# Optimization experiments

Hardware: AMD Instinct MI355X
Metric: run time of the kernel (lower is better)

The kernel has to match this reference:

```python
import jax, jax.numpy as jnp
import numpy as np


def _gcn_conv(x, src, dst, dis, W, b, num_nodes):
    # x: [N, Fin]; src/dst: [E+N] (self-loops included); dis: [N] deg^{-1/2}
    h = x @ W                                   # [N, Fout] dense transform first (Fin >= Fout)
    norm = dis[src] * dis[dst]                  # [E+N] symmetric GCN normalization
    msg = h[src] * norm[:, None]                # gather + scale
    out = jax.ops.segment_sum(msg, dst, num_segments=num_nodes)  # scatter-add at targets
    return out + b


def setup_inputs() -> dict:
    key = jax.random.key(0)
    k1, k2, k3, k4 = jax.random.split(key, 4)
    N, F, H, C, E = 100000, 512, 32, 32, 3200000
    x = jax.random.normal(k1, (N, F), dtype=jnp.float32)
    edge_index = jax.random.randint(k2, (2, E), 0, N, dtype=jnp.int64)
    W1 = jax.random.normal(k3, (F, H), dtype=jnp.float32) * (1.0 / np.sqrt(F))
    b1 = jnp.zeros((H,), dtype=jnp.float32)
    W2 = jax.random.normal(k4, (H, C), dtype=jnp.float32) * (1.0 / np.sqrt(H))
    b2 = jnp.zeros((C,), dtype=jnp.float32)
    return {"x": x, "edge_index": edge_index, "W1": W1, "b1": b1, "W2": W2, "b2": b2}


def reference(x, edge_index, W1, b1, W2, b2):
    N = x.shape[0]
    loop = jnp.arange(N, dtype=edge_index.dtype)
    src = jnp.concatenate([edge_index[0], loop])   # add self-loops (PyG default)
    dst = jnp.concatenate([edge_index[1], loop])
    deg = jax.ops.segment_sum(jnp.ones_like(dst, dtype=x.dtype), dst, num_segments=N)
    dis = jnp.where(deg > 0, jax.lax.rsqrt(jnp.maximum(deg, 1.0)), 0.0)  # deg^{-1/2}, 0 for isolated
    h = _gcn_conv(x, src, dst, dis, W1, b1, N)
    h = jax.nn.relu(h)                              # dropout is identity in eval mode
    h = _gcn_conv(h, src, dst, dis, W2, b2, N)
    return jax.nn.log_softmax(h, axis=1)
```

## Files before the change

### kernel.cpp

```cpp
#include <hip/hip_runtime.h>
#include <hip/hip_bf16.h>

#define FIN 512
#define HD 32
#define BNODES 512
#define CH 8192
#define NHB 128

typedef short s16x8 __attribute__((ext_vector_type(8)));
typedef float f32x4 __attribute__((ext_vector_type(4)));

__device__ inline unsigned short f2b(float f) {
  unsigned u = __float_as_uint(f);
  return (unsigned short)((u + 0x7FFFu + ((u >> 16) & 1u)) >> 16);
}
__device__ inline float b2f(unsigned short b) {
  return __uint_as_float((unsigned)b << 16);
}
__device__ inline float b2f_lo(unsigned u) { return __uint_as_float(u << 16); }
__device__ inline float b2f_hi(unsigned u) { return __uint_as_float(u & 0xFFFF0000u); }

__global__ __launch_bounds__(256) void k_bktcnt(const int* __restrict__ dst, int* __restrict__ hist, int E) {
  __shared__ int h[256];
  int t = threadIdx.x;
  h[t] = 0;
  __syncthreads();
  for (int i = blockIdx.x * 256 + t; i < E; i += gridDim.x * 256)
    atomicAdd(&h[dst[i] >> 9], 1);
  __syncthreads();
  hist[blockIdx.x * 256 + t] = h[t];
}

__global__ __launch_bounds__(256) void k_bscan(const int* __restrict__ hist, int* __restrict__ bcnt,
                                               int* __restrict__ bbase, int* __restrict__ bfill) {
  __shared__ int s[256];
  int t = threadIdx.x;
  int v = 0;
  for (int b = 0; b < NHB; ++b) v += hist[b * 256 + t];
  bcnt[t] = v;
  s[t] = v;
  __syncthreads();
  for (int o = 1; o < 256; o <<= 1) {
    int a = (t >= o) ? s[t - o] : 0;
    __syncthreads();
    s[t] += a;
    __syncthreads();
  }
  bbase[t] = s[t] - v;
  bfill[t] = s[t] - v;
}

__global__ __launch_bounds__(512) void k_bin(const int* __restrict__ src, const int* __restrict__ dst,
                                             int* __restrict__ bfill, int* __restrict__ bin, int E) {
  __shared__ int raw[CH];
  __shared__ unsigned char bkt[CH];
  __shared__ int cnt[256];
  __shared__ int gbase[256];
  int t = threadIdx.x;
  for (int cb = blockIdx.x * CH; cb < E; cb += gridDim.x * CH) {
    int n = E - cb; if (n > CH) n = CH;
    if (t < 256) cnt[t] = 0;
    __syncthreads();
    for (int j = t; j < n; j += 512) {
      int s = src[cb + j], d = dst[cb + j];
      raw[j] = s | ((d & 511) << 22);
      bkt[j] = (unsigned char)(d >> 9);
      atomicAdd(&cnt[d >> 9], 1);
    }
    __syncthreads();
    if (t < 256) {
      int c = cnt[t];
      gbase[t] = (c > 0) ? atomicAdd(&bfill[t], c) : 0;
      cnt[t] = 0;
    }
    __syncthreads();
    for (int j = t; j < n; j += 512) {
      int b = bkt[j];
      int r = atomicAdd(&cnt[b], 1);
      bin[gbase[b] + r] = raw[j];
    }
    __syncthreads();
  }
}

__global__ __launch_bounds__(512) void k_csr(const int* __restrict__ bin, const int* __restrict__ bbase,
                                             const int* __restrict__ bcnt, int* __restrict__ cntm1,
                                             float* __restrict__ dis, int* __restrict__ offsets,
                                             int* __restrict__ csr, int N) {
  __shared__ int cnt[BNODES];
  __shared__ int sc[BNODES];
  const int t = threadIdx.x;
  const int bkt = blockIdx.x;
  const int n0 = bkt * BNODES;
  int nn = N - n0; if (nn > BNODES) nn = BNODES;
  const int eb = bbase[bkt], ec = bcnt[bkt];

  cnt[t] = 0;
  __syncthreads();
  for (int j = t; j < ec; j += 512)
    atomicAdd(&cnt[(unsigned)bin[eb + j] >> 22], 1);
  __syncthreads();
  int v = cnt[t];
  if (t < nn) {
    cntm1[n0 + t] = v;
    dis[n0 + t] = rsqrtf((float)(v + 1));
  }
  sc[t] = v;
  __syncthreads();
  for (int o = 1; o < 512; o <<= 1) {
    int a = (t >= o) ? sc[t - o] : 0;
    __syncthreads();
    sc[t] += a;
    __syncthreads();
  }
  int myoff = sc[t] - v;
  if (t < nn) offsets[n0 + t] = eb + myoff;
  cnt[t] = myoff;
  __syncthreads();
  for (int j = t; j < ec; j += 512) {
    int e = bin[eb + j];
    int pos = atomicAdd(&cnt[(unsigned)e >> 22], 1);
    csr[eb + pos] = e & 0x3FFFFF;
  }
}

#define XPAD 72
#define WPAD 520
__global__ __launch_bounds__(512) void k_mm1(const float* __restrict__ x, const float* __restrict__ W1,
                                             const float* __restrict__ dis, unsigned short* __restrict__ h1b,
                                             int N) {
  __shared__ unsigned short wT[32 * WPAD];
  __shared__ unsigned short xs[128 * XPAD];
  const int t = threadIdx.x;
  const int rbase = blockIdx.x * 128;

  for (int idx = t; idx < FIN * HD; idx += 512) {
    int k = idx >> 5, c = idx & 31;
    wT[c * WPAD + k] = f2b(W1[idx]);
  }

  const int lane = t & 63;
  const int wrow = (t >> 6) * 16;
  const int m16 = lane & 15;
  const int kg = lane >> 4;

  f32x4 acc0 = {0.f, 0.f, 0.f, 0.f};
  f32x4 acc1 = {0.f, 0.f, 0.f, 0.f};

  for (int kc = 0; kc < FIN; kc += 64) {
    __syncthreads();
#pragma unroll
    for (int p = 0; p < 4; ++p) {
      int idx = p * 512 + t;
      int r = idx >> 4, kq = idx & 15;
      int grow = rbase + r;
      float4 v = (grow < N) ? *(const float4*)&x[(size_t)grow * FIN + kc + kq * 4]
                            : make_float4(0.f, 0.f, 0.f, 0.f);
      unsigned p0 = (unsigned)f2b(v.x) | ((unsigned)f2b(v.y) << 16);
      unsigned p1 = (unsigned)f2b(v.z) | ((unsigned)f2b(v.w) << 16);
      *(uint2*)&xs[r * XPAD + kq * 4] = make_uint2(p0, p1);
    }
    __syncthreads();

    s16x8 a0  = *(const s16x8*)&xs[(wrow + m16) * XPAD + kg * 8];
    s16x8 a1  = *(const s16x8*)&xs[(wrow + m16) * XPAD + 32 + kg * 8];
    s16x8 b00 = *(const s16x8*)&wT[m16 * WPAD + kc + kg * 8];
    s16x8 b01 = *(const s16x8*)&wT[(16 + m16) * WPAD + kc + kg * 8];
    s16x8 b10 = *(const s16x8*)&wT[m16 * WPAD + kc + 32 + kg * 8];
    s16x8 b11 = *(const s16x8*)&wT[(16 + m16) * WPAD + kc + 32 + kg * 8];
    acc0 = __builtin_amdgcn_mfma_f32_16x16x32_bf16(a0, b00, acc0, 0, 0, 0);
    acc1 = __builtin_amdgcn_mfma_f32_16x16x32_bf16(a0, b01, acc1, 0, 0, 0);
    acc0 = __builtin_amdgcn_mfma_f32_16x16x32_bf16(a1, b10, acc0, 0, 0, 0);
    acc1 = __builtin_amdgcn_mfma_f32_16x16x32_bf16(a1, b11, acc1, 0, 0, 0);
  }

#pragma unroll
  for (int r = 0; r < 4; ++r) {
    int row = rbase + wrow + kg * 4 + r;
    if (row < N) {
      float dr = dis[row];
      h1b[(size_t)row * HD + m16]      = f2b(acc0[r] * dr);
      h1b[(size_t)row * HD + 16 + m16] = f2b(acc1[r] * dr);
    }
  }
}

__device__ inline float pull_row(const unsigned short* __restrict__ h, const int* __restrict__ csr,
                                 int jb, int cnt, int L, int es, int cg) {
  float a0 = 0.f, a1 = 0.f, a2 = 0.f, a3 = 0.f, a4 = 0.f, a5 = 0.f, a6 = 0.f, a7 = 0.f;
  for (int j = 0; j < cnt; j += 8) {
    int eidx = j + es;
    int sidx = csr[jb + min(eidx, cnt - 1)];
    uint4 u = *(const uint4*)&h[(size_t)sidx * HD + cg * 8];
    if (eidx >= cnt) u = make_uint4(0, 0, 0, 0);
    a0 += b2f_lo(u.x); a1 += b2f_hi(u.x);
    a2 += b2f_lo(u.y); a3 += b2f_hi(u.y);
    a4 += b2f_lo(u.z); a5 += b2f_hi(u.z);
    a6 += b2f_lo(u.w); a7 += b2f_hi(u.w);
  }
#pragma unroll
  for (int o = 4; o <= 16; o <<= 1) {
    a0 += __shfl_xor(a0, o, 32); a1 += __shfl_xor(a1, o, 32);
    a2 += __shfl_xor(a2, o, 32); a3 += __shfl_xor(a3, o, 32);
    a4 += __shfl_xor(a4, o, 32); a5 += __shfl_xor(a5, o, 32);
    a6 += __shfl_xor(a6, o, 32); a7 += __shfl_xor(a7, o, 32);
  }
  int srcl = L >> 3;
  int sel = L & 7;
  float sum = __shfl(a0, srcl, 32);
  float c1 = __shfl(a1, srcl, 32); sum = (sel == 1) ? c1 : sum;
  float c2 = __shfl(a2, srcl, 32); sum = (sel == 2) ? c2 : sum;
  float c3 = __shfl(a3, srcl, 32); sum = (sel == 3) ? c3 : sum;
  float c4 = __shfl(a4, srcl, 32); sum = (sel == 4) ? c4 : sum;
  float c5 = __shfl(a5, srcl, 32); sum = (sel == 5) ? c5 : sum;
  float c6 = __shfl(a6, srcl, 32); sum = (sel == 6) ? c6 : sum;
  float c7 = __shfl(a7, srcl, 32); sum = (sel == 7) ? c7 : sum;
  return sum;
}

__global__ __launch_bounds__(256) void k_pull1_mm2(const unsigned short* __restrict__ h1b,
                                                   const int* __restrict__ csr, const int* __restrict__ offsets,
                                                   const int* __restrict__ cntm1, const float* __restrict__ dis,
                                                   const float* __restrict__ b1, const float* __restrict__ W2,
                                                   unsigned short* __restrict__ h2b, int N) {
  __shared__ float w[HD * HD];
  __shared__ float bb[HD];
  int t = threadIdx.x;
  if (t < HD) bb[t] = b1[t];
  for (int i = t; i < HD * HD; i += 256) w[i] = W2[i];
  __syncthreads();

  int lane = t & 63, L = lane & 31;
  int es = L >> 2, cg = L & 3;
  int halfId = (blockIdx.x * 4 + (t >> 6)) * 2 + (lane >> 5);
  int stride = gridDim.x * 8;
  for (int i = halfId; i < N; i += stride) {
    float sum = pull_row(h1b, csr, offsets[i], cntm1[i], L, es, cg);
    float self = b2f(h1b[(size_t)i * HD + L]);
    float d = dis[i];
    float tv = fmaxf(fmaf(d, sum + self, bb[L]), 0.f);
    float a2 = 0.f;
#pragma unroll
    for (int k = 0; k < HD; ++k) a2 = fmaf(__shfl(tv, k, 32), w[k * HD + L], a2);
    h2b[(size_t)i * HD + L] = f2b(a2 * d);
  }
}

__global__ __launch_bounds__(256) void k_pull2_lsm(const unsigned short* __restrict__ h2b,
                                                   const int* __restrict__ csr, const int* __restrict__ offsets,
                                                   const int* __restrict__ cntm1, const float* __restrict__ dis,
                                                   const float* __restrict__ b2, float* __restrict__ out, int N) {
  __shared__ float bb[HD];
  int t = threadIdx.x;
  if (t < HD) bb[t] = b2[t];
  __syncthreads();

  int lane = t & 63, L = lane & 31;
  int es = L >> 2, cg = L & 3;
  int halfId = (blockIdx.x * 4 + (t >> 6)) * 2 + (lane >> 5);
  int stride = gridDim.x * 8;
  for (int i = halfId; i < N; i += stride) {
    float sum = pull_row(h2b, csr, offsets[i], cntm1[i], L, es, cg);
    float self = b2f(h2b[(size_t)i * HD + L]);
    float v = fmaf(dis[i], sum + self, bb[L]);
    float m = v;
    for (int off = 16; off; off >>= 1) m = fmaxf(m, __shfl_xor(m, off, 32));
    float ex = __expf(v - m);
    float sm = ex;
    for (int off = 16; off; off >>= 1) sm += __shfl_xor(sm, off, 32);
    out[(size_t)i * HD + L] = v - m - __logf(sm);
  }
}

extern "C" void kernel_launch(void* const* d_in, const int* in_sizes, int n_in,
                              void* d_out, int out_size, void* d_ws, size_t ws_size,
                              hipStream_t stream) {
  const float* x  = (const float*)d_in[0];
  const int*   ei = (const int*)d_in[1];
  const float* W1 = (const float*)d_in[2];
  const float* b1 = (const float*)d_in[3];
  const float* W2 = (const float*)d_in[4];
  const float* b2 = (const float*)d_in[5];
  float* out = (float*)d_out;

  const int H   = in_sizes[3];
  const int Fin = in_sizes[2] / H;
  const int N   = in_sizes[0] / Fin;
  const int E   = in_sizes[1] / 2;
  const int* src = ei;
  const int* dst = ei + E;
  const int B   = (N + BNODES - 1) / BNODES;

  char* wsp = (char*)d_ws;
  size_t off = 0;
  auto nxt = [&](size_t bytes) { char* p = wsp + off; off = (off + bytes + 255) & ~(size_t)255; return p; };
  int*   hist    = (int*)  nxt((size_t)NHB * 256 * 4);
  int*   bcnt    = (int*)  nxt(256 * 4);
  int*   bbase   = (int*)  nxt(256 * 4);
  int*   bfill   = (int*)  nxt(256 * 4);
  int*   cntm1   = (int*)  nxt((size_t)N * 4);
  float* dis     = (float*)nxt((size_t)N * 4);
  int*   offsets = (int*)  nxt((size_t)N * 4);
  int*   bin     = (int*)  nxt((size_t)E * 4);
  int*   csr     = (int*)  nxt((size_t)E * 4);
  unsigned short* h1b = (unsigned short*)nxt((size_t)N * HD * 2);
  unsigned short* h2b = (unsigned short*)nxt((size_t)N * HD * 2);
  (void)ws_size; (void)n_in; (void)out_size;

  k_bktcnt<<<NHB, 256, 0, stream>>>(dst, hist, E);
  k_bscan<<<1, 256, 0, stream>>>(hist, bcnt, bbase, bfill);
  k_bin<<<(E + CH - 1) / CH, 512, 0, stream>>>(src, dst, bfill, bin, E);
  k_csr<<<B, 512, 0, stream>>>(bin, bbase, bcnt, cntm1, dis, offsets, csr, N);
  k_mm1<<<(N + 127) / 128, 512, 0, stream>>>(x, W1, dis, h1b, N);
  k_pull1_mm2<<<2048, 256, 0, stream>>>(h1b, csr, offsets, cntm1, dis, b1, W2, h2b, N);
  k_pull2_lsm<<<2048, 256, 0, stream>>>(h2b, csr, offsets, cntm1, dis, b2, out, N);
}
```

Baseline: 259.4 us.

## Overlap edge binning with the first GEMM and split layer-2 transform into MFMA kernel

Binning blocks and mm1 blocks now share one launch, so the x@W1 GEMM no longer waits for the degree computation and the bandwidth-heavy x read overlaps the binning atomics. Scaling by deg^-1/2 moves into k_csr, which rewrites the unscaled h1 into a scaled copy. The per-lane shuffle-based 32x32 W2 multiply in pull1 is replaced by a separate bf16 MFMA kernel reading an intermediate buffer. This costs extra global round-trips for h1u and tt, an extra launch, and a larger shared-memory footprint for the binning blocks.

```diff
diff --git a/kernel.cpp b/kernel.cpp
--- a/kernel.cpp
+++ b/kernel.cpp
@@ -50,21 +50,29 @@
   bfill[t] = s[t] - v;
 }
 
-__global__ __launch_bounds__(512) void k_bin(const int* __restrict__ src, const int* __restrict__ dst,
-                                             int* __restrict__ bfill, int* __restrict__ bin, int E) {
-  __shared__ int raw[CH];
-  __shared__ unsigned char bkt[CH];
-  __shared__ int cnt[256];
-  __shared__ int gbase[256];
-  int t = threadIdx.x;
-  for (int cb = blockIdx.x * CH; cb < E; cb += gridDim.x * CH) {
+#define XPAD 72
+#define WPAD 520
+#define SMEM_BYTES 51712
+__global__ __launch_bounds__(512) void k_fused(const int* __restrict__ src, const int* __restrict__ dst,
+                                               int* __restrict__ bfill, int* __restrict__ bin, int E, int NBIN,
+                                               const float* __restrict__ x, const float* __restrict__ W1,
+                                               unsigned short* __restrict__ h1u, int N) {
+  __shared__ __align__(16) char smem[SMEM_BYTES];
+  const int t = threadIdx.x;
+
+  if (blockIdx.x < NBIN) {
+    int* raw = (int*)smem;
+    unsigned short* bkt = (unsigned short*)(smem + 32768);
+    int* cnt = (int*)(smem + 49152);
+    int* gbase = (int*)(smem + 50176);
+    int cb = blockIdx.x * CH;
     int n = E - cb; if (n > CH) n = CH;
     if (t < 256) cnt[t] = 0;
     __syncthreads();
     for (int j = t; j < n; j += 512) {
       int s = src[cb + j], d = dst[cb + j];
       raw[j] = s | ((d & 511) << 22);
-      bkt[j] = (unsigned char)(d >> 9);
+      bkt[j] = (unsigned short)(d >> 9);
       atomicAdd(&cnt[d >> 9], 1);
     }
     __syncthreads();
@@ -79,16 +87,70 @@
       int r = atomicAdd(&cnt[b], 1);
       bin[gbase[b] + r] = raw[j];
     }
-    __syncthreads();
+  } else {
+    unsigned short* wT = (unsigned short*)smem;
+    unsigned short* xs = (unsigned short*)(smem + 33280);
+    const int rbase = (blockIdx.x - NBIN) * 128;
+
+    for (int idx = t; idx < FIN * HD; idx += 512) {
+      int k = idx >> 5, c = idx & 31;
+      wT[c * WPAD + k] = f2b(W1[idx]);
+    }
+
+    const int lane = t & 63;
+    const int wrow = (t >> 6) * 16;
+    const int m16 = lane & 15;
+    const int kg = lane >> 4;
+
+    f32x4 acc0 = {0.f, 0.f, 0.f, 0.f};
+    f32x4 acc1 = {0.f, 0.f, 0.f, 0.f};
+
+    for (int kc = 0; kc < FIN; kc += 64) {
+      __syncthreads();
+#pragma unroll
+      for (int p = 0; p < 4; ++p) {
+        int idx = p * 512 + t;
+        int r = idx >> 4, kq = idx & 15;
+        int grow = rbase + r;
+        float4 v = (grow < N) ? *(const float4*)&x[(size_t)grow * FIN + kc + kq * 4]
+                              : make_float4(0.f, 0.f, 0.f, 0.f);
+        unsigned p0 = (unsigned)f2b(v.x) | ((unsigned)f2b(v.y) << 16);
+        unsigned p1 = (unsigned)f2b(v.z) | ((unsigned)f2b(v.w) << 16);
+        *(uint2*)&xs[r * XPAD + kq * 4] = make_uint2(p0, p1);
+      }
+      __syncthreads();
+
+      s16x8 a0  = *(const s16x8*)&xs[(wrow + m16) * XPAD + kg * 8];
+      s16x8 a1  = *(const s16x8*)&xs[(wrow + m16) * XPAD + 32 + kg * 8];
+      s16x8 b00 = *(const s16x8*)&wT[m16 * WPAD + kc + kg * 8];
+      s16x8 b01 = *(const s16x8*)&wT[(16 + m16) * WPAD + kc + kg * 8];
+      s16x8 b10 = *(const s16x8*)&wT[m16 * WPAD + kc + 32 + kg * 8];
+      s16x8 b11 = *(const s16x8*)&wT[(16 + m16) * WPAD + kc + 32 + kg * 8];
+      acc0 = __builtin_amdgcn_mfma_f32_16x16x32_bf16(a0, b00, acc0, 0, 0, 0);
+      acc1 = __builtin_amdgcn_mfma_f32_16x16x32_bf16(a0, b01, acc1, 0, 0, 0);
+      acc0 = __builtin_amdgcn_mfma_f32_16x16x32_bf16(a1, b10, acc0, 0, 0, 0);
+      acc1 = __builtin_amdgcn_mfma_f32_16x16x32_bf16(a1, b11, acc1, 0, 0, 0);
+    }
+
+#pragma unroll
+    for (int r = 0; r < 4; ++r) {
+      int row = rbase + wrow + kg * 4 + r;
+      if (row < N) {
+        h1u[(size_t)row * HD + m16]      = f2b(acc0[r]);
+        h1u[(size_t)row * HD + 16 + m16] = f2b(acc1[r]);
+      }
+    }
   }
 }
 
 __global__ __launch_bounds__(512) void k_csr(const int* __restrict__ bin, const int* __restrict__ bbase,
                                              const int* __restrict__ bcnt, int* __restrict__ cntm1,
                                              float* __restrict__ dis, int* __restrict__ offsets,
-                                             int* __restrict__ csr, int N) {
+                                             int* __restrict__ csr, const unsigned short* __restrict__ h1u,
+                                             unsigned short* __restrict__ h1b, int N) {
   __shared__ int cnt[BNODES];
   __shared__ int sc[BNODES];
+  __shared__ float disl[BNODES];
   const int t = threadIdx.x;
   const int bkt = blockIdx.x;
   const int n0 = bkt * BNODES;
@@ -101,9 +163,11 @@
     atomicAdd(&cnt[(unsigned)bin[eb + j] >> 22], 1);
   __syncthreads();
   int v = cnt[t];
+  float dv = rsqrtf((float)(v + 1));
   if (t < nn) {
     cntm1[n0 + t] = v;
-    dis[n0 + t] = rsqrtf((float)(v + 1));
+    dis[n0 + t] = dv;
+    disl[t] = dv;
   }
   sc[t] = v;
   __syncthreads();
@@ -122,72 +186,21 @@
     int pos = atomicAdd(&cnt[(unsigned)e >> 22], 1);
     csr[eb + pos] = e & 0x3FFFFF;
   }
-}
-
-#define XPAD 72
-#define WPAD 520
-__global__ __launch_bounds__(512) void k_mm1(const float* __restrict__ x, const float* __restrict__ W1,
-                                             const float* __restrict__ dis, unsigned short* __restrict__ h1b,
-                                             int N) {
-  __shared__ unsigned short wT[32 * WPAD];
-  __shared__ unsigned short xs[128 * XPAD];
-  const int t = threadIdx.x;
-  const int rbase = blockIdx.x * 128;
-
-  for (int idx = t; idx < FIN * HD; idx += 512) {
-    int k = idx >> 5, c = idx & 31;
-    wT[c * WPAD + k] = f2b(W1[idx]);
-  }
-
-  const int lane = t & 63;
-  const int wrow = (t >> 6) * 16;
-  const int m16 = lane & 15;
-  const int kg = lane >> 4;
-
-  f32x4 acc0 = {0.f, 0.f, 0.f, 0.f};
-  f32x4 acc1 = {0.f, 0.f, 0.f, 0.f};
-
-  for (int kc = 0; kc < FIN; kc += 64) {
-    __syncthreads();
-#pragma unroll
-    for (int p = 0; p < 4; ++p) {
-      int idx = p * 512 + t;
-      int r = idx >> 4, kq = idx & 15;
-      int grow = rbase + r;
-      float4 v = (grow < N) ? *(const float4*)&x[(size_t)grow * FIN + kc + kq * 4]
-                            : make_float4(0.f, 0.f, 0.f, 0.f);
-      unsigned p0 = (unsigned)f2b(v.x) | ((unsigned)f2b(v.y) << 16);
-      unsigned p1 = (unsigned)f2b(v.z) | ((unsigned)f2b(v.w) << 16);
-      *(uint2*)&xs[r * XPAD + kq * 4] = make_uint2(p0, p1);
-    }
-    __syncthreads();
-
-    s16x8 a0  = *(const s16x8*)&xs[(wrow + m16) * XPAD + kg * 8];
-    s16x8 a1  = *(const s16x8*)&xs[(wrow + m16) * XPAD + 32 + kg * 8];
-    s16x8 b00 = *(const s16x8*)&wT[m16 * WPAD + kc + kg * 8];
-    s16x8 b01 = *(const s16x8*)&wT[(16 + m16) * WPAD + kc + kg * 8];
-    s16x8 b10 = *(const s16x8*)&wT[m16 * WPAD + kc + 32 + kg * 8];
-    s16x8 b11 = *(const s16x8*)&wT[(16 + m16) * WPAD + kc + 32 + kg * 8];
-    acc0 = __builtin_amdgcn_mfma_f32_16x16x32_bf16(a0, b00, acc0, 0, 0, 0);
-    acc1 = __builtin_amdgcn_mfma_f32_16x16x32_bf16(a0, b01, acc1, 0, 0, 0);
-    acc0 = __builtin_amdgcn_mfma_f32_16x16x32_bf16(a1, b10, acc0, 0, 0, 0);
-    acc1 = __builtin_amdgcn_mfma_f32_16x16x32_bf16(a1, b11, acc1, 0, 0, 0);
-  }
-
-#pragma unroll
-  for (int r = 0; r < 4; ++r) {
-    int row = rbase + wrow + kg * 4 + r;
-    if (row < N) {
-      float dr = dis[row];
-      h1b[(size_t)row * HD + m16]      = f2b(acc0[r] * dr);
-      h1b[(size_t)row * HD + 16 + m16] = f2b(acc1[r] * dr);
-    }
-  }
-}
-
-__device__ inline float pull_row(const unsigned short* __restrict__ h, const int* __restrict__ csr,
-                                 int jb, int cnt, int L, int es, int cg) {
-  float a0 = 0.f, a1 = 0.f, a2 = 0.f, a3 = 0.f, a4 = 0.f, a5 = 0.f, a6 = 0.f, a7 = 0.f;
+  const unsigned* hu = (const unsigned*)(h1u + (size_t)n0 * HD);
+  unsigned* hb = (unsigned*)(h1b + (size_t)n0 * HD);
+  int total = nn * (HD / 2);
+  for (int i = t; i < total; i += 512) {
+    int r = i >> 4;
+    float d = disl[r];
+    unsigned u = hu[i];
+    hb[i] = (unsigned)f2b(b2f_lo(u) * d) | ((unsigned)f2b(b2f_hi(u) * d) << 16);
+  }
+}
+
+__device__ inline void gather8(const unsigned short* __restrict__ h, const int* __restrict__ csr,
+                               int jb, int cnt, int es, int cg,
+                               float& a0, float& a1, float& a2, float& a3,
+                               float& a4, float& a5, float& a6, float& a7) {
   for (int j = 0; j < cnt; j += 8) {
     int eidx = j + es;
     int sidx = csr[jb + min(eidx, cnt - 1)];
@@ -205,29 +218,16 @@
     a4 += __shfl_xor(a4, o, 32); a5 += __shfl_xor(a5, o, 32);
     a6 += __shfl_xor(a6, o, 32); a7 += __shfl_xor(a7, o, 32);
   }
-  int srcl = L >> 3;
-  int sel = L & 7;
-  float sum = __shfl(a0, srcl, 32);
-  float c1 = __shfl(a1, srcl, 32); sum = (sel == 1) ? c1 : sum;
-  float c2 = __shfl(a2, srcl, 32); sum = (sel == 2) ? c2 : sum;
-  float c3 = __shfl(a3, srcl, 32); sum = (sel == 3) ? c3 : sum;
-  float c4 = __shfl(a4, srcl, 32); sum = (sel == 4) ? c4 : sum;
-  float c5 = __shfl(a5, srcl, 32); sum = (sel == 5) ? c5 : sum;
-  float c6 = __shfl(a6, srcl, 32); sum = (sel == 6) ? c6 : sum;
-  float c7 = __shfl(a7, srcl, 32); sum = (sel == 7) ? c7 : sum;
-  return sum;
-}
-
-__global__ __launch_bounds__(256) void k_pull1_mm2(const unsigned short* __restrict__ h1b,
-                                                   const int* __restrict__ csr, const int* __restrict__ offsets,
-                                                   const int* __restrict__ cntm1, const float* __restrict__ dis,
-                                                   const float* __restrict__ b1, const float* __restrict__ W2,
-                                                   unsigned short* __restrict__ h2b, int N) {
-  __shared__ float w[HD * HD];
+}
+
+__global__ __launch_bounds__(256) void k_pull1(const unsigned short* __restrict__ h1b,
+                                               const int* __restrict__ csr, const int* __restrict__ offsets,
+                                               const int* __restrict__ cntm1, const float* __restrict__ dis,
+                                               const float* __restrict__ b1, unsigned short* __restrict__ tt,
+                                               int N) {
   __shared__ float bb[HD];
   int t = threadIdx.x;
   if (t < HD) bb[t] = b1[t];
-  for (int i = t; i < HD * HD; i += 256) w[i] = W2[i];
   __syncthreads();
 
   int lane = t & 63, L = lane & 31;
@@ -235,14 +235,65 @@
   int halfId = (blockIdx.x * 4 + (t >> 6)) * 2 + (lane >> 5);
   int stride = gridDim.x * 8;
   for (int i = halfId; i < N; i += stride) {
-    float sum = pull_row(h1b, csr, offsets[i], cntm1[i], L, es, cg);
-    float self = b2f(h1b[(size_t)i * HD + L]);
-    float d = dis[i];
-    float tv = fmaxf(fmaf(d, sum + self, bb[L]), 0.f);
-    float a2 = 0.f;
+    float a0 = 0.f, a1 = 0.f, a2 = 0.f, a3 = 0.f, a4 = 0.f, a5 = 0.f, a6 = 0.f, a7 = 0.f;
+    gather8(h1b, csr, offsets[i], cntm1[i], es, cg, a0, a1, a2, a3, a4, a5, a6, a7);
+    if (L < 4) {
+      uint4 su = *(const uint4*)&h1b[(size_t)i * HD + cg * 8];
+      float d = dis[i];
+      const float* bp = &bb[cg * 8];
+      float v0 = fmaxf(fmaf(d, a0 + b2f_lo(su.x), bp[0]), 0.f);
+      float v1 = fmaxf(fmaf(d, a1 + b2f_hi(su.x), bp[1]), 0.f);
+      float v2 = fmaxf(fmaf(d, a2 + b2f_lo(su.y), bp[2]), 0.f);
+      float v3 = fmaxf(fmaf(d, a3 + b2f_hi(su.y), bp[3]), 0.f);
+      float v4 = fmaxf(fmaf(d, a4 + b2f_lo(su.z), bp[4]), 0.f);
+      float v5 = fmaxf(fmaf(d, a5 + b2f_hi(su.z), bp[5]), 0.f);
+      float v6 = fmaxf(fmaf(d, a6 + b2f_lo(su.w), bp[6]), 0.f);
+      float v7 = fmaxf(fmaf(d, a7 + b2f_hi(su.w), bp[7]), 0.f);
+      uint4 pk;
+      pk.x = (unsigned)f2b(v0) | ((unsigned)f2b(v1) << 16);
+      pk.y = (unsigned)f2b(v2) | ((unsigned)f2b(v3) << 16);
+      pk.z = (unsigned)f2b(v4) | ((unsigned)f2b(v5) << 16);
+      pk.w = (unsigned)f2b(v6) | ((unsigned)f2b(v7) << 16);
+      *(uint4*)&tt[(size_t)i * HD + cg * 8] = pk;
+    }
+  }
+}
+
+#define WP2 36
+__global__ __launch_bounds__(512) void k_mm2(const unsigned short* __restrict__ tt,
+                                             const float* __restrict__ W2, const float* __restrict__ dis,
+                                             unsigned short* __restrict__ h2b, int N) {
+  __shared__ unsigned short wT2[32 * WP2];
+  const int t = threadIdx.x;
+  const int rbase = blockIdx.x * 128;
+  for (int idx = t; idx < HD * HD; idx += 512) {
+    int k = idx >> 5, c = idx & 31;
+    wT2[c * WP2 + k] = f2b(W2[idx]);
+  }
+  __syncthreads();
+
+  const int lane = t & 63;
+  const int wrow = (t >> 6) * 16;
+  const int m16 = lane & 15;
+  const int kg = lane >> 4;
+
+  int arow = rbase + wrow + m16;
+  s16x8 a = {0, 0, 0, 0, 0, 0, 0, 0};
+  if (arow < N) a = *(const s16x8*)&tt[(size_t)arow * HD + kg * 8];
+  s16x8 b0 = *(const s16x8*)&wT2[m16 * WP2 + kg * 8];
+  s16x8 b1 = *(const s16x8*)&wT2[(16 + m16) * WP2 + kg * 8];
+  f32x4 z = {0.f, 0.f, 0.f, 0.f};
+  f32x4 acc0 = __builtin_amdgcn_mfma_f32_16x16x32_bf16(a, b0, z, 0, 0, 0);
+  f32x4 acc1 = __builtin_amdgcn_mfma_f32_16x16x32_bf16(a, b1, z, 0, 0, 0);
+
 #pragma unroll
-    for (int k = 0; k < HD; ++k) a2 = fmaf(__shfl(tv, k, 32), w[k * HD + L], a2);
-    h2b[(size_t)i * HD + L] = f2b(a2 * d);
+  for (int r = 0; r < 4; ++r) {
+    int row = rbase + wrow + kg * 4 + r;
+    if (row < N) {
+      float dr = dis[row];
+      h2b[(size_t)row * HD + m16]      = f2b(acc0[r] * dr);
+      h2b[(size_t)row * HD + 16 + m16] = f2b(acc1[r] * dr);
+    }
   }
 }
 
@@ -260,9 +311,22 @@
   int halfId = (blockIdx.x * 4 + (t >> 6)) * 2 + (lane >> 5);
   int stride = gridDim.x * 8;
   for (int i = halfId; i < N; i += stride) {
-    float sum = pull_row(h2b, csr, offsets[i], cntm1[i], L, es, cg);
-    float self = b2f(h2b[(size_t)i * HD + L]);
-    float v = fmaf(dis[i], sum + self, bb[L]);
+    float a0 = 0.f, a1 = 0.f, a2 = 0.f, a3 = 0.f, a4 = 0.f, a5 = 0.f, a6 = 0.f, a7 = 0.f;
+    gather8(h2b, csr, offsets[i], cntm1[i], es, cg, a0, a1, a2, a3, a4, a5, a6, a7);
+    int srcl = L >> 3;
+    int sel = L & 7;
+    float sum = __shfl(a0, srcl, 32);
+    float c;
+    c = __shfl(a1, srcl, 32); sum = (sel == 1) ? c : sum;
+    c = __shfl(a2, srcl, 32); sum = (sel == 2) ? c : sum;
+    c = __shfl(a3, srcl, 32); sum = (sel == 3) ? c : sum;
+    c = __shfl(a4, srcl, 32); sum = (sel == 4) ? c : sum;
+    c = __shfl(a5, srcl, 32); sum = (sel == 5) ? c : sum;
+    c = __shfl(a6, srcl, 32); sum = (sel == 6) ? c : sum;
+    c = __shfl(a7, srcl, 32); sum = (sel == 7) ? c : sum;
+
+    sum += b2f(h2b[(size_t)i * HD + L]);
+    float v = fmaf(dis[i], sum, bb[L]);
     float m = v;
     for (int off = 16; off; off >>= 1) m = fmaxf(m, __shfl_xor(m, off, 32));
     float ex = __expf(v - m);
@@ -289,7 +353,9 @@
   const int E   = in_sizes[1] / 2;
   const int* src = ei;
   const int* dst = ei + E;
-  const int B   = (N + BNODES - 1) / BNODES;
+  const int B    = (N + BNODES - 1) / BNODES;
+  const int NBIN = (E + CH - 1) / CH;
+  const int NMM1 = (N + 127) / 128;
 
   char* wsp = (char*)d_ws;
   size_t off = 0;
@@ -303,15 +369,17 @@
   int*   offsets = (int*)  nxt((size_t)N * 4);
   int*   bin     = (int*)  nxt((size_t)E * 4);
   int*   csr     = (int*)  nxt((size_t)E * 4);
+  unsigned short* h1u = (unsigned short*)nxt((size_t)N * HD * 2);
   unsigned short* h1b = (unsigned short*)nxt((size_t)N * HD * 2);
+  unsigned short* tt  = (unsigned short*)nxt((size_t)N * HD * 2);
   unsigned short* h2b = (unsigned short*)nxt((size_t)N * HD * 2);
   (void)ws_size; (void)n_in; (void)out_size;
 
   k_bktcnt<<<NHB, 256, 0, stream>>>(dst, hist, E);
   k_bscan<<<1, 256, 0, stream>>>(hist, bcnt, bbase, bfill);
-  k_bin<<<(E + CH - 1) / CH, 512, 0, stream>>>(src, dst, bfill, bin, E);
-  k_csr<<<B, 512, 0, stream>>>(bin, bbase, bcnt, cntm1, dis, offsets, csr, N);
-  k_mm1<<<(N + 127) / 128, 512, 0, stream>>>(x, W1, dis, h1b, N);
-  k_pull1_mm2<<<2048, 256, 0, stream>>>(h1b, csr, offsets, cntm1, dis, b1, W2, h2b, N);
+  k_fused<<<NBIN + NMM1, 512, 0, stream>>>(src, dst, bfill, bin, E, NBIN, x, W1, h1u, N);
+  k_csr<<<B, 512, 0, stream>>>(bin, bbase, bcnt, cntm1, dis, offsets, csr, h1u, h1b, N);
+  k_pull1<<<2048, 256, 0, stream>>>(h1b, csr, offsets, cntm1, dis, b1, tt, N);
+  k_mm2<<<NMM1, 512, 0, stream>>>(tt, W2, dis, h2b, N);
   k_pull2_lsm<<<2048, 256, 0, stream>>>(h2b, csr, offsets, cntm1, dis, b2, out, N);
 }
```

New measurement: 230.2 us. 1.13x faster.
